# Kernel tuning notes

Hardware: AMD Instinct MI355X
Metric: run time of the kernel (lower is better)

Reference implementation:

```python
import jax, jax.numpy as jnp
import numpy as np

N_NODES = 50000
N_EDGES = 1600000
IN_CH = 128
OUT_CH = 64
HEADS = 2
NEG_SLOPE = 0.2


def setup_inputs() -> dict:
    key = jax.random.key(0)
    ks = jax.random.split(key, 9)
    return {
        "x": jax.random.normal(ks[0], (N_NODES, IN_CH), dtype=jnp.float32),
        "embedding": jax.random.normal(ks[1], (N_NODES, OUT_CH), dtype=jnp.float32),
        "lin_w": jax.random.normal(ks[2], (IN_CH, HEADS * OUT_CH), dtype=jnp.float32) * (1.0 / np.sqrt(IN_CH)),
        "att_i": jax.random.normal(ks[3], (HEADS, OUT_CH), dtype=jnp.float32) * 0.1,
        "att_j": jax.random.normal(ks[4], (HEADS, OUT_CH), dtype=jnp.float32) * 0.1,
        "att_em_i": jax.random.normal(ks[5], (HEADS, OUT_CH), dtype=jnp.float32) * 0.1,
        "att_em_j": jax.random.normal(ks[6], (HEADS, OUT_CH), dtype=jnp.float32) * 0.1,
        "edge_src": jax.random.randint(ks[7], (N_EDGES,), 0, N_NODES, dtype=jnp.int64 if jax.config.read("jax_enable_x64") else jnp.int32),
        "edge_dst": jax.random.randint(ks[8], (N_EDGES,), 0, N_NODES, dtype=jnp.int64 if jax.config.read("jax_enable_x64") else jnp.int32),
    }


def reference(x, embedding, lin_w, att_i, att_j, att_em_i, att_em_j, edge_src, edge_dst):
    N = x.shape[0]
    H, D = att_i.shape
    # linear projection: [N, H, D]
    xh = (x @ lin_w).reshape(N, H, D)
    # add self loops
    loop = jnp.arange(N, dtype=edge_src.dtype)
    src = jnp.concatenate([edge_src, loop])
    dst = jnp.concatenate([edge_dst, loop])
    # per-node attention scores (cat(x, emb) . cat(att, att_em) split into two dots)
    s_i = jnp.einsum("nhd,hd->nh", xh, att_i) + embedding @ att_em_i.T  # [N,H]
    s_j = jnp.einsum("nhd,hd->nh", xh, att_j) + embedding @ att_em_j.T  # [N,H]
    # per-edge attention: x_i is src feature, x_j is dst feature (as in source)
    alpha = jax.nn.leaky_relu(s_i[src] + s_j[dst], negative_slope=NEG_SLOPE)  # [E+N,H]
    alpha = jax.nn.softmax(alpha, axis=1)  # softmax over heads, per the source code
    # message is alpha * x[dst]; aggregated at dst => x[n] * sum of alpha over incoming edges
    w = jax.ops.segment_sum(alpha, dst, num_segments=N)  # [N,H]
    out = xh * w[:, :, None]  # [N,H,D]
    return out.mean(axis=1)  # [N,D]
```

## Files before the change

kernel.cpp:

```cpp
#include <hip/hip_runtime.h>
#include <hip/hip_bf16.h>

#define IN_CH 128
#define OUT_CH 64
#define NEG_SLOPE 0.2f
#define KPACK 1024.5f

#define BSHIFT 8
#define CHUNK 8192
#define NGEMM 256
#define CAPMAX 9216
#define FIX20 1048576.0f

typedef short bf16x8 __attribute__((ext_vector_type(8)));
typedef float f32x4 __attribute__((ext_vector_type(4)));
typedef unsigned long long u64;
typedef unsigned int u32;

__device__ __forceinline__ unsigned short f2bf(float f) {
  union { float f; unsigned u; } v;
  v.f = f;
  unsigned r = v.u + 0x7FFF + ((v.u >> 16) & 1);
  return (unsigned short)(r >> 16);
}

__global__ __launch_bounds__(256) void prep_kernel(
    const float* __restrict__ lw, const float* __restrict__ att_i,
    const float* __restrict__ att_j, float* __restrict__ u,
    int* __restrict__ gcur) {
  const int tid = threadIdx.x;
  const int which = blockIdx.x;
  if (which == 0) gcur[tid] = 0;
  const float* att = which ? att_j : att_i;
  int k = tid & 127;
  int h = (tid >> 7) & 1;
  float v = 0.f;
#pragma unroll 8
  for (int d = 0; d < 64; ++d)
    v = fmaf(lw[(size_t)k * IN_CH + h * 64 + d], att[h * 64 + d], v);
  u[which * 256 + h * 128 + k] = v;
}

__global__ __launch_bounds__(256) void score_kernel(
    const float* __restrict__ x, const float* __restrict__ emb,
    const float* __restrict__ u, const float* __restrict__ aei,
    const float* __restrict__ aej, float2* __restrict__ si,
    float2* __restrict__ sj, float* __restrict__ wself,
    float* __restrict__ wsum, int N) {
  const int tid = threadIdx.x;
  const int wave = tid >> 6;
  const int lane = tid & 63;
  const int n = blockIdx.x * 4 + wave;
  if (n >= N) return;

  float x0 = x[(size_t)n * IN_CH + lane];
  float x1 = x[(size_t)n * IN_CH + 64 + lane];
  float em = emb[(size_t)n * OUT_CH + lane];

  float v_si0 = fmaf(x0, u[lane], fmaf(x1, u[64 + lane], em * aei[lane]));
  float v_si1 =
      fmaf(x0, u[128 + lane], fmaf(x1, u[192 + lane], em * aei[64 + lane]));
  float v_sj0 =
      fmaf(x0, u[256 + lane], fmaf(x1, u[320 + lane], em * aej[lane]));
  float v_sj1 =
      fmaf(x0, u[384 + lane], fmaf(x1, u[448 + lane], em * aej[64 + lane]));

#pragma unroll
  for (int off = 32; off > 0; off >>= 1) {
    v_si0 += __shfl_xor(v_si0, off, 64);
    v_si1 += __shfl_xor(v_si1, off, 64);
    v_sj0 += __shfl_xor(v_sj0, off, 64);
    v_sj1 += __shfl_xor(v_sj1, off, 64);
  }

  if (lane == 0) {
    si[n] = make_float2(v_si0, v_si1);
    sj[n] = make_float2(v_sj0, v_sj1);
    float a0 = v_si0 + v_sj0;
    float a1 = v_si1 + v_sj1;
    a0 = a0 > 0.f ? a0 : NEG_SLOPE * a0;
    a1 = a1 > 0.f ? a1 : NEG_SLOPE * a1;
    wself[n] = 1.f / (1.f + __expf(a1 - a0));
    wsum[n] = 0.f;
  }
}

__global__ __launch_bounds__(256) void bin_gemm_kernel(
    const float* __restrict__ x, const float* __restrict__ lw,
    const int* __restrict__ esrc, const int* __restrict__ edst,
    const float2* __restrict__ si, const float2* __restrict__ sj,
    float* __restrict__ xh, float* __restrict__ wsum,
    u32* __restrict__ brecs, int* __restrict__ gcur, int cap, int nbin, int N,
    int E) {
  __shared__ __align__(16) u64 smem8[4352];
  __shared__ int hist[256];
  __shared__ int scan[256];
  __shared__ int gbase[256];
  __shared__ int cur[256];
  const int bid = blockIdx.x;
  const int tid = threadIdx.x;
  const int wave = tid >> 6;
  const int lane = tid & 63;

  if (bid < nbin) {
    u32* recs = (u32*)smem8;

    hist[tid] = 0;
    __syncthreads();

    const long e0 = (long)bid * CHUNK;
    const int cnt = (int)min((long)CHUNK, (long)E - e0);

    for (int r = tid; r < cnt; r += 256)
      atomicAdd(&hist[edst[e0 + r] >> BSHIFT], 1);
    __syncthreads();

    scan[tid] = hist[tid];
    __syncthreads();
#pragma unroll
    for (int ofs = 1; ofs < 256; ofs <<= 1) {
      int t = (tid >= ofs) ? scan[tid - ofs] : 0;
      __syncthreads();
      scan[tid] += t;
      __syncthreads();
    }
    int excl = scan[tid] - hist[tid];
    __syncthreads();
    scan[tid] = excl;
    cur[tid] = excl;
    gbase[tid] = (hist[tid] > 0) ? atomicAdd(&gcur[tid], hist[tid]) : 0;
    __syncthreads();

    for (int r = tid; r < cnt; r += 256) {
      long e = e0 + r;
      int s = esrc[e];
      int d = edst[e];
      float2 aa = si[s];
      float2 bb = sj[d];
      float a0 = aa.x + bb.x;
      float a1 = aa.y + bb.y;
      a0 = a0 > 0.f ? a0 : NEG_SLOPE * a0;
      a1 = a1 > 0.f ? a1 : NEG_SLOPE * a1;
      float p0 = 1.f / (1.f + __expf(a1 - a0));
      u32 fx = (u32)fminf(p0 * FIX20 + 0.5f, 1048575.0f);
      int pos = atomicAdd(&cur[d >> BSHIFT], 1);
      recs[pos] = ((u32)(d & 255) << 20) | fx;
    }
    __syncthreads();

    for (int b = wave; b < 256; b += 4) {
      int c = hist[b];
      int s0 = scan[b];
      int g0 = gbase[b];
      u32* dp = brecs + (size_t)b * cap;
      int base = (b << BSHIFT) & ~255;
      for (int r = lane; r < c; r += 64) {
        u32 rec = recs[s0 + r];
        int gofs = g0 + r;
        if (gofs < cap) {
          dp[gofs] = rec;
        } else {
          float p0 = (float)(rec & 0xFFFFF) * (1.0f / FIX20);
          unsafeAtomicAdd(&wsum[base + (int)(rec >> 20)], KPACK + p0);
        }
      }
    }
  } else {
    typedef unsigned short BlRow[136];
    BlRow* Bl = (BlRow*)smem8;
    const int g = bid - nbin;

    for (int i = tid; i < IN_CH * IN_CH; i += 256) {
      int k = i >> 7;
      int c = i & 127;
      Bl[c][k] = f2bf(lw[i]);
    }
    __syncthreads();

    const int ntiles = (N + 63) / 64;
    const int ko = (lane >> 4) * 8;
    const int ccol = lane & 15;
    for (int tile = g; tile < ntiles; tile += NGEMM) {
      const int row0 = tile * 64 + wave * 16;
      int arow = row0 + (lane & 15);
      if (arow >= N) arow = N - 1;
      const float* ap = x + (size_t)arow * IN_CH + ko;
      bf16x8 a[4];
#pragma unroll
      for (int kb = 0; kb < 4; ++kb) {
        float4 f0 = *(const float4*)(ap + kb * 32);
        float4 f1 = *(const float4*)(ap + kb * 32 + 4);
        bf16x8 t;
        t[0] = (short)f2bf(f0.x); t[1] = (short)f2bf(f0.y);
        t[2] = (short)f2bf(f0.z); t[3] = (short)f2bf(f0.w);
        t[4] = (short)f2bf(f1.x); t[5] = (short)f2bf(f1.y);
        t[6] = (short)f2bf(f1.z); t[7] = (short)f2bf(f1.w);
        a[kb] = t;
      }
      const int crow0 = row0 + (lane >> 4) * 4;
#pragma unroll
      for (int nt = 0; nt < 8; ++nt) {
        f32x4 acc = {0.f, 0.f, 0.f, 0.f};
        const bf16x8* bp = (const bf16x8*)&Bl[nt * 16 + ccol][ko];
        acc = __builtin_amdgcn_mfma_f32_16x16x32_bf16(a[0], bp[0], acc, 0, 0, 0);
        acc = __builtin_amdgcn_mfma_f32_16x16x32_bf16(a[1], bp[4], acc, 0, 0, 0);
        acc = __builtin_amdgcn_mfma_f32_16x16x32_bf16(a[2], bp[8], acc, 0, 0, 0);
        acc = __builtin_amdgcn_mfma_f32_16x16x32_bf16(a[3], bp[12], acc, 0, 0, 0);
#pragma unroll
        for (int rr = 0; rr < 4; ++rr) {
          int n = crow0 + rr;
          if (n < N) xh[(size_t)n * IN_CH + nt * 16 + ccol] = acc[rr];
        }
      }
    }
  }
}

__global__ __launch_bounds__(1024) void reduce_out_kernel(
    const float* __restrict__ xh, const float* __restrict__ wsum,
    const float* __restrict__ wself, const u32* __restrict__ brecs,
    const int* __restrict__ gcur, int cap, float* __restrict__ out, int N) {
  __shared__ u64 table[256];
  const int b = blockIdx.x;
  const int tid = threadIdx.x;

  if (tid < 256) table[tid] = 0ull;
  __syncthreads();

  const int cnt = min(gcur[b], cap);
  const u32* rp = brecs + (size_t)b * cap;
  for (int r = tid; r < cnt; r += 1024) {
    u32 rec = rp[r];
    atomicAdd(&table[rec >> 20], (1ull << 32) | (u64)(rec & 0xFFFFF));
  }
  __syncthreads();

  const int n0 = b << BSHIFT;
  const int nmax = min(256, N - n0);
  for (int t = tid; t < nmax * 16; t += 1024) {
    int ln = t >> 4;
    int n = n0 + ln;
    int c4 = (t & 15) << 2;
    u64 acc = table[ln];
    float cnt_i = (float)(u32)(acc >> 32);
    float s0_i = (float)(u32)(acc & 0xFFFFFFFFu) * (1.0f / FIX20);
    float wsv = wsum[n];
    float cnt_s = floorf(wsv * (1.0f / KPACK));
    float s0_s = wsv - KPACK * cnt_s;
    float p0s = wself[n];
    float w0 = s0_i + s0_s + p0s;
    float w1 = (cnt_i + cnt_s - s0_i - s0_s) + (1.f - p0s);
    float4 v0 = *(const float4*)&xh[(size_t)n * IN_CH + c4];
    float4 v1 = *(const float4*)&xh[(size_t)n * IN_CH + 64 + c4];
    float4 o;
    o.x = 0.5f * fmaf(v0.x, w0, v1.x * w1);
    o.y = 0.5f * fmaf(v0.y, w0, v1.y * w1);
    o.z = 0.5f * fmaf(v0.z, w0, v1.z * w1);
    o.w = 0.5f * fmaf(v0.w, w0, v1.w * w1);
    *(float4*)&out[(size_t)n * OUT_CH + c4] = o;
  }
}

extern "C" void kernel_launch(void* const* d_in, const int* in_sizes, int n_in,
                              void* d_out, int out_size, void* d_ws,
                              size_t ws_size, hipStream_t stream) {
  const float* x = (const float*)d_in[0];
  const float* emb = (const float*)d_in[1];
  const float* lw = (const float*)d_in[2];
  const float* att_i = (const float*)d_in[3];
  const float* att_j = (const float*)d_in[4];
  const float* aei = (const float*)d_in[5];
  const float* aej = (const float*)d_in[6];
  const int* esrc = (const int*)d_in[7];
  const int* edst = (const int*)d_in[8];
  float* out = (float*)d_out;

  int N = in_sizes[0] / IN_CH;
  int E = in_sizes[7];
  int nb = (N + 255) >> BSHIFT;
  int nbin = (E + CHUNK - 1) / CHUNK;

  char* ws = (char*)d_ws;
  float* xh = (float*)ws;
  float2* si = (float2*)(ws + (size_t)N * IN_CH * 4);
  float2* sj = si + N;
  float* wself = (float*)(sj + N);
  float* wsum = wself + N;
  float* u = wsum + N;
  int* gcur = (int*)(u + 512);
  u32* brecs = (u32*)(gcur + 256);

  size_t fixed = (size_t)((char*)brecs - ws);
  size_t avail = ws_size > fixed ? (ws_size - fixed) / 4 : 0;
  int cap = (int)(avail / (nb > 0 ? nb : 1));
  if (cap > CAPMAX) cap = CAPMAX;
  if (cap < 1024) cap = 1024;

  prep_kernel<<<dim3(2), dim3(256), 0, stream>>>(lw, att_i, att_j, u, gcur);
  score_kernel<<<dim3((N + 3) / 4), dim3(256), 0, stream>>>(
      x, emb, u, aei, aej, si, sj, wself, wsum, N);
  bin_gemm_kernel<<<dim3(nbin + NGEMM), dim3(256), 0, stream>>>(
      x, lw, esrc, edst, si, sj, xh, wsum, brecs, gcur, cap, nbin, N, E);
  reduce_out_kernel<<<dim3(nb), dim3(1024), 0, stream>>>(
      xh, wsum, wself, brecs, gcur, cap, out, N);
}
```

Baseline: 167.0 us.

## Precompute bf16 transposed weights and shrink bin chunks to cut LDS use

The bf16 transpose of lin_w now happens once in prep_kernel into workspace, so GEMM blocks read B fragments from global/L2 instead of each block rebuilding a 34KB LDS copy. Shared memory in the binning kernel drops to a 16KB record buffer, and CHUNK is halved with more GEMM blocks, which allows higher occupancy and more binning blocks. The flush loop is rewritten to flatten records across threads using a binary search over the scan, replacing per-wave bucket loops that were imbalanced. The trade-off is that B loads go to global memory without LDS reuse, and each flushed record now costs a search.

```diff
diff --git a/kernel.cpp b/kernel.cpp
--- a/kernel.cpp
+++ b/kernel.cpp
@@ -7,8 +7,8 @@
 #define KPACK 1024.5f
 
 #define BSHIFT 8
-#define CHUNK 8192
-#define NGEMM 256
+#define CHUNK 4096
+#define NGEMM 391
 #define CAPMAX 9216
 #define FIX20 1048576.0f
 
@@ -26,19 +26,27 @@
 
 __global__ __launch_bounds__(256) void prep_kernel(
     const float* __restrict__ lw, const float* __restrict__ att_i,
-    const float* __restrict__ att_j, float* __restrict__ u,
-    int* __restrict__ gcur) {
+    const float* __restrict__ att_j, unsigned short* __restrict__ lwt,
+    float* __restrict__ u, int* __restrict__ gcur) {
+  const int bid = blockIdx.x;
   const int tid = threadIdx.x;
-  const int which = blockIdx.x;
-  if (which == 0) gcur[tid] = 0;
-  const float* att = which ? att_j : att_i;
-  int k = tid & 127;
-  int h = (tid >> 7) & 1;
-  float v = 0.f;
+  if (bid == 0) gcur[tid] = 0;
+  if (bid < 64) {
+    int idx = bid * 256 + tid;
+    int k = idx >> 7;
+    int c = idx & 127;
+    lwt[(size_t)c * IN_CH + k] = f2bf(lw[idx]);
+  } else {
+    int which = bid - 64;
+    const float* att = which ? att_j : att_i;
+    int k = tid & 127;
+    int h = (tid >> 7) & 1;
+    float v = 0.f;
 #pragma unroll 8
-  for (int d = 0; d < 64; ++d)
-    v = fmaf(lw[(size_t)k * IN_CH + h * 64 + d], att[h * 64 + d], v);
-  u[which * 256 + h * 128 + k] = v;
+    for (int d = 0; d < 64; ++d)
+      v = fmaf(lw[(size_t)k * IN_CH + h * 64 + d], att[h * 64 + d], v);
+    u[which * 256 + h * 128 + k] = v;
+  }
 }
 
 __global__ __launch_bounds__(256) void score_kernel(
@@ -86,13 +94,13 @@
 }
 
 __global__ __launch_bounds__(256) void bin_gemm_kernel(
-    const float* __restrict__ x, const float* __restrict__ lw,
+    const float* __restrict__ x, const unsigned short* __restrict__ lwt,
     const int* __restrict__ esrc, const int* __restrict__ edst,
     const float2* __restrict__ si, const float2* __restrict__ sj,
     float* __restrict__ xh, float* __restrict__ wsum,
     u32* __restrict__ brecs, int* __restrict__ gcur, int cap, int nbin, int N,
     int E) {
-  __shared__ __align__(16) u64 smem8[4352];
+  __shared__ u32 recs[CHUNK];
   __shared__ int hist[256];
   __shared__ int scan[256];
   __shared__ int gbase[256];
@@ -103,8 +111,6 @@
   const int lane = tid & 63;
 
   if (bid < nbin) {
-    u32* recs = (u32*)smem8;
-
     hist[tid] = 0;
     __syncthreads();
 
@@ -148,35 +154,25 @@
     }
     __syncthreads();
 
-    for (int b = wave; b < 256; b += 4) {
-      int c = hist[b];
-      int s0 = scan[b];
-      int g0 = gbase[b];
-      u32* dp = brecs + (size_t)b * cap;
-      int base = (b << BSHIFT) & ~255;
-      for (int r = lane; r < c; r += 64) {
-        u32 rec = recs[s0 + r];
-        int gofs = g0 + r;
-        if (gofs < cap) {
-          dp[gofs] = rec;
-        } else {
-          float p0 = (float)(rec & 0xFFFFF) * (1.0f / FIX20);
-          unsafeAtomicAdd(&wsum[base + (int)(rec >> 20)], KPACK + p0);
-        }
+    for (int p = tid; p < cnt; p += 256) {
+      int lo = 0, hi = 255;
+#pragma unroll
+      for (int it = 0; it < 8; ++it) {
+        int mid = (lo + hi + 1) >> 1;
+        if (scan[mid] <= p) lo = mid; else hi = mid - 1;
+      }
+      int b = lo;
+      int gofs = gbase[b] + (p - scan[b]);
+      u32 rec = recs[p];
+      if (gofs < cap) {
+        brecs[(size_t)b * cap + gofs] = rec;
+      } else {
+        float p0 = (float)(rec & 0xFFFFF) * (1.0f / FIX20);
+        unsafeAtomicAdd(&wsum[(b << BSHIFT) + (int)(rec >> 20)], KPACK + p0);
       }
     }
   } else {
-    typedef unsigned short BlRow[136];
-    BlRow* Bl = (BlRow*)smem8;
     const int g = bid - nbin;
-
-    for (int i = tid; i < IN_CH * IN_CH; i += 256) {
-      int k = i >> 7;
-      int c = i & 127;
-      Bl[c][k] = f2bf(lw[i]);
-    }
-    __syncthreads();
-
     const int ntiles = (N + 63) / 64;
     const int ko = (lane >> 4) * 8;
     const int ccol = lane & 15;
@@ -201,7 +197,8 @@
 #pragma unroll
       for (int nt = 0; nt < 8; ++nt) {
         f32x4 acc = {0.f, 0.f, 0.f, 0.f};
-        const bf16x8* bp = (const bf16x8*)&Bl[nt * 16 + ccol][ko];
+        const bf16x8* bp =
+            (const bf16x8*)(lwt + (size_t)(nt * 16 + ccol) * IN_CH + ko);
         acc = __builtin_amdgcn_mfma_f32_16x16x32_bf16(a[0], bp[0], acc, 0, 0, 0);
         acc = __builtin_amdgcn_mfma_f32_16x16x32_bf16(a[1], bp[4], acc, 0, 0, 0);
         acc = __builtin_amdgcn_mfma_f32_16x16x32_bf16(a[2], bp[8], acc, 0, 0, 0);
@@ -287,7 +284,8 @@
   float* wself = (float*)(sj + N);
   float* wsum = wself + N;
   float* u = wsum + N;
-  int* gcur = (int*)(u + 512);
+  unsigned short* lwt = (unsigned short*)(u + 512);
+  int* gcur = (int*)(lwt + 16384);
   u32* brecs = (u32*)(gcur + 256);
 
   size_t fixed = (size_t)((char*)brecs - ws);
@@ -296,11 +294,12 @@
   if (cap > CAPMAX) cap = CAPMAX;
   if (cap < 1024) cap = 1024;
 
-  prep_kernel<<<dim3(2), dim3(256), 0, stream>>>(lw, att_i, att_j, u, gcur);
+  prep_kernel<<<dim3(66), dim3(256), 0, stream>>>(lw, att_i, att_j, lwt, u,
+                                                  gcur);
   score_kernel<<<dim3((N + 3) / 4), dim3(256), 0, stream>>>(
       x, emb, u, aei, aej, si, sj, wself, wsum, N);
   bin_gemm_kernel<<<dim3(nbin + NGEMM), dim3(256), 0, stream>>>(
-      x, lw, esrc, edst, si, sj, xh, wsum, brecs, gcur, cap, nbin, N, E);
+      x, lwt, esrc, edst, si, sj, xh, wsum, brecs, gcur, cap, nbin, N, E);
   reduce_out_kernel<<<dim3(nb), dim3(1024), 0, stream>>>(
       xh, wsum, wself, brecs, gcur, cap, out, N);
 }
```

After: 163.7 us. Within noise of the previous version (-1.9%).
